# Optimization experiments

Measured on AMD Instinct MI355X. Metric: run time of the kernel, lower is better.

The kernel has to match this reference:

```python
import jax, jax.numpy as jnp
import numpy as np

N_MESH = 10242
N_GRID = 65160
N_EDGES = 195480
D = 512          # latent dim for mesh/grid nodes and edges
OUT = 471        # out_grid_node_dim
EDGE_IN = 4      # raw mesh2grid edge attribute dim


def _mlp(x, w0, b0, w1, b1):
    # MLP(in, hidden, out) with one hidden layer and SiLU (swish) activation, as in GraphCast
    return jax.nn.silu(x @ w0 + b0) @ w1 + b1


def setup_inputs() -> dict:
    key = jax.random.key(0)
    ks = jax.random.split(key, 24)
    s = 0.05  # weight scale to keep activations sane
    inp = {
        "mesh_node_features": jax.random.normal(ks[0], (1, N_MESH, D), jnp.float32),
        "grid_node_features": jax.random.normal(ks[1], (1, N_GRID, D), jnp.float32),
        "edge_attrs": jax.random.normal(ks[2], (N_EDGES, EDGE_IN), jnp.float32),
        "edge_src": jax.random.randint(ks[3], (N_EDGES,), 0, N_MESH),
        "edge_dst": jax.random.randint(ks[4], (N_EDGES,), 0, N_GRID),
        # edge embedder: 4 -> 512 -> 512
        "emb_w0": jax.random.normal(ks[5], (EDGE_IN, D)) * s,
        "emb_b0": jnp.zeros((D,)),
        "emb_w1": jax.random.normal(ks[6], (D, D)) * s,
        "emb_b1": jnp.zeros((D,)),
        # processor edge MLP: [src(512) + dst(512) + edge(512)] -> 512 -> 512
        "edge_w0": jax.random.normal(ks[7], (3 * D, D)) * s,
        "edge_b0": jnp.zeros((D,)),
        "edge_w1": jax.random.normal(ks[8], (D, D)) * s,
        "edge_b1": jnp.zeros((D,)),
        # processor node MLP: [grid(512) + agg(512)] -> 512 -> 512
        "node_w0": jax.random.normal(ks[9], (2 * D, D)) * s,
        "node_b0": jnp.zeros((D,)),
        "node_w1": jax.random.normal(ks[10], (D, D)) * s,
        "node_b1": jnp.zeros((D,)),
        # output MLP: 512 -> 512 -> 471
        "out_w0": jax.random.normal(ks[11], (D, D)) * s,
        "out_b0": jnp.zeros((D,)),
        "out_w1": jax.random.normal(ks[12], (D, OUT)) * s,
        "out_b1": jnp.zeros((OUT,)),
    }
    return inp


def reference(mesh_node_features, grid_node_features, edge_attrs, edge_src, edge_dst,
              emb_w0, emb_b0, emb_w1, emb_b1,
              edge_w0, edge_b0, edge_w1, edge_b1,
              node_w0, node_b0, node_w1, node_b1,
              out_w0, out_b0, out_w1, out_b1):
    B = grid_node_features.shape[0]
    # 1) embed raw edge attributes [E,4] -> [E,D]
    e = _mlp(edge_attrs, emb_w0, emb_b0, emb_w1, emb_b1)
    e = jnp.broadcast_to(e[None], (B, N_EDGES, D))  # [B,E,D]
    # 2) one message-passing step (InteractionNetwork style, residual)
    src = mesh_node_features[:, edge_src]  # gather: [B,E,D]
    dst = grid_node_features[:, edge_dst]  # gather: [B,E,D]
    e_in = jnp.concatenate([src, dst, e], axis=-1)  # [B,E,3D]
    e = e + _mlp(e_in, edge_w0, edge_b0, edge_w1, edge_b1)  # residual edge update
    # scatter-sum messages onto destination grid nodes
    agg = jax.vmap(lambda ef: jax.ops.segment_sum(ef, edge_dst, num_segments=N_GRID))(e)  # [B,N_GRID,D]
    n_in = jnp.concatenate([grid_node_features, agg], axis=-1)  # [B,N_GRID,2D]
    grid = grid_node_features + _mlp(n_in, node_w0, node_b0, node_w1, node_b1)  # residual node update
    # 3) output MLP (no layernorm)
    out = _mlp(grid, out_w0, out_b0, out_w1, out_b1)  # [B,N_GRID,OUT]
    return out.astype(jnp.float32)
```

## Files before the change

kernel.cpp:

```cpp
#include <hip/hip_runtime.h>
#include <stdint.h>

#define NE 195480
#define NM 10242
#define NG 65160
#define DD 512
#define NOUT 471

typedef __attribute__((ext_vector_type(8))) short bf16x8;
typedef __attribute__((ext_vector_type(4))) float f32x4;
typedef __attribute__((ext_vector_type(8))) unsigned short ushort8;

__device__ __forceinline__ float bf2f(unsigned short u) {
    union { unsigned int i; float f; } v; v.i = ((unsigned int)u) << 16; return v.f;
}
__device__ __forceinline__ unsigned short f2bf(float f) {
    union { float f; unsigned int u; } v; v.f = f;
    unsigned int x = v.u;
    return (unsigned short)((x + 0x7fffu + ((x >> 16) & 1u)) >> 16);
}
__device__ __forceinline__ float silu_f(float x) { return x / (1.f + __expf(-x)); }

__device__ __forceinline__ ushort8 cvt8(const float* __restrict__ p) {
    const f32x4 lo = *(const f32x4*)p;
    const f32x4 hi = *(const f32x4*)(p + 4);
    ushort8 r;
    #pragma unroll
    for (int j = 0; j < 4; ++j) { r[j] = f2bf(lo[j]); r[j + 4] = f2bf(hi[j]); }
    return r;
}

__device__ __forceinline__ void gl_lds16(const unsigned short* g, unsigned short* l) {
    __builtin_amdgcn_global_load_lds(
        (const __attribute__((address_space(1))) unsigned int*)g,
        (__attribute__((address_space(3))) unsigned int*)l, 16, 0, 0);
}

enum { A_PLAIN = 0, A_SEG = 1 };
enum { E_BIAS_BF16 = 0, E_SILU_BF16 = 1, E_AGGSILU = 2, E_OUT_F32 = 3 };

template<int AMODE, int EPI>
__global__ __launch_bounds__(256)
void gemm128(const unsigned short* __restrict__ Asrc,
             const unsigned short* __restrict__ Asrc2,
             const unsigned short* __restrict__ Asrc3,
             const unsigned short* __restrict__ Bw,
             const float* __restrict__ bias,
             const float* __restrict__ bias2,
             int M, int N, int K, int ldOut,
             const unsigned* __restrict__ degA,
             unsigned short* __restrict__ outB,
             float* __restrict__ outF)
{
    __shared__ unsigned short As[128 * 64];
    __shared__ unsigned short Bs[128 * 64];

    const int tid  = threadIdx.x;
    const int nwg  = gridDim.x;
    int orig = blockIdx.x;
    if ((nwg & 7) == 0) {
        const int q = nwg >> 3;
        orig = (blockIdx.x & 7) * q + (blockIdx.x >> 3);
    }
    const int bn = orig & 3;
    const int bm = orig >> 2;

    const int w    = tid >> 6;
    const int lane = tid & 63;
    const int quad = lane >> 4;
    const int ln   = lane & 15;
    const int wr   = w >> 1;
    const int wc   = w & 1;

    const int srow = tid >> 3;
    const int sc   = tid & 7;
    const int ck   = (sc ^ (srow & 7)) * 8;

    int arowc[4];
    #pragma unroll
    for (int i = 0; i < 4; ++i) {
        int r = bm * 128 + i * 32 + srow;
        arowc[i] = (r < M) ? r : (M - 1);
    }

    f32x4 acc[4][4] = {};

    for (int k0 = 0; k0 < K; k0 += 64) {
        __syncthreads();
        #pragma unroll
        for (int i = 0; i < 4; ++i) {
            const int row = i * 32 + srow;
            const unsigned short* ga;
            if (AMODE == A_PLAIN) {
                ga = Asrc + (size_t)arowc[i] * K + k0 + ck;
            } else {
                if (k0 < 512)       ga = Asrc  + (size_t)arowc[i] * 512 + k0 + ck;
                else if (k0 < 1024) ga = Asrc2 + (size_t)arowc[i] * 512 + (k0 - 512) + ck;
                else                ga = Asrc3 + (size_t)arowc[i] * 512 + (k0 - 1024) + ck;
            }
            gl_lds16(ga, As + i * 2048 + tid * 8);
            gl_lds16(Bw + (size_t)(bn * 128 + row) * K + k0 + ck, Bs + i * 2048 + tid * 8);
        }
        __syncthreads();

        #pragma unroll
        for (int kt = 0; kt < 2; ++kt) {
            bf16x8 af[4], bfv[4];
            #pragma unroll
            for (int m = 0; m < 4; ++m) {
                const int r = wr * 64 + m * 16 + ln;
                af[m] = *(const bf16x8*)(As + r * 64 + (((kt * 4 + quad) ^ (r & 7)) * 8));
            }
            #pragma unroll
            for (int n = 0; n < 4; ++n) {
                const int r = wc * 64 + n * 16 + ln;
                bfv[n] = *(const bf16x8*)(Bs + r * 64 + (((kt * 4 + quad) ^ (r & 7)) * 8));
            }
            #pragma unroll
            for (int m = 0; m < 4; ++m)
                #pragma unroll
                for (int n = 0; n < 4; ++n)
                    acc[m][n] = __builtin_amdgcn_mfma_f32_16x16x32_bf16(af[m], bfv[n], acc[m][n], 0, 0, 0);
        }
    }

    int colg[4]; float bcol[4], bcol2[4]; bool cok[4];
    #pragma unroll
    for (int n = 0; n < 4; ++n) {
        colg[n] = bn * 128 + wc * 64 + n * 16 + ln;
        cok[n]  = (colg[n] < N);
        bcol[n] = cok[n] ? bias[colg[n]] : 0.f;
        bcol2[n] = (EPI == E_AGGSILU && cok[n]) ? bias2[colg[n]] : 0.f;
    }
    #pragma unroll
    for (int m = 0; m < 4; ++m) {
        #pragma unroll
        for (int r = 0; r < 4; ++r) {
            const int row_g = bm * 128 + wr * 64 + m * 16 + quad * 4 + r;
            if (row_g >= M) continue;
            const float deg = (EPI == E_AGGSILU) ? (float)degA[row_g] : 0.f;
            #pragma unroll
            for (int n = 0; n < 4; ++n) {
                if (!cok[n]) continue;
                float v = acc[m][n][r] + bcol[n];
                if (EPI == E_BIAS_BF16) {
                    outB[(size_t)row_g * ldOut + colg[n]] = f2bf(v);
                } else if (EPI == E_SILU_BF16) {
                    outB[(size_t)row_g * ldOut + colg[n]] = f2bf(silu_f(v));
                } else if (EPI == E_AGGSILU) {
                    outB[(size_t)row_g * ldOut + colg[n]] = f2bf(silu_f(v + deg * bcol2[n]));
                } else {
                    outF[(size_t)row_g * N + colg[n]] = v;
                }
            }
        }
    }
}

__global__ __launch_bounds__(256)
void wconv(const float* __restrict__ w, unsigned short* __restrict__ wT,
           int K, int N, int Npad, int ldT)
{
    __shared__ float t[64][65];
    const int tid = threadIdx.x;
    const int bk = blockIdx.x * 64, bn = blockIdx.y * 64;
    const int cc = tid & 63, rr = tid >> 6;
    #pragma unroll
    for (int i = 0; i < 16; ++i) {
        const int k = rr + i * 4;
        float v = 0.f;
        if (bk + k < K && bn + cc < N) v = w[(size_t)(bk + k) * N + bn + cc];
        t[k][cc] = v;
    }
    __syncthreads();
    #pragma unroll
    for (int i = 0; i < 16; ++i) {
        const int n = rr + i * 4;
        if (bn + n < Npad && bk + cc < K)
            wT[(size_t)(bn + n) * ldT + bk + cc] = f2bf(t[cc][n]);
    }
}

__global__ __launch_bounds__(256)
void cvtb(const float* __restrict__ in, unsigned short* __restrict__ out, long long n8)
{
    const long long i = (long long)blockIdx.x * 256 + threadIdx.x;
    if (i >= n8) return;
    *(ushort8*)(out + i * 8) = cvt8(in + i * 8);
}

__global__ __launch_bounds__(256)
void embed_l1(const float* __restrict__ attrs,
              const float* __restrict__ w0,
              const float* __restrict__ b0,
              unsigned short* __restrict__ h)
{
    const long long idx = (long long)blockIdx.x * 256 + threadIdx.x;
    if (idx >= (long long)NE * 512) return;
    const int row = (int)(idx >> 9);
    const int c = (int)(idx & 511);
    float acc = b0[c];
    #pragma unroll
    for (int k = 0; k < 4; ++k)
        acc += attrs[row * 4 + k] * w0[k * 512 + c];
    h[idx] = f2bf(silu_f(acc));
}

__global__ __launch_bounds__(256)
void esilu(unsigned short* __restrict__ z,
           const unsigned short* __restrict__ mP,
           const unsigned short* __restrict__ gP,
           const int* __restrict__ esrc,
           const int* __restrict__ edst)
{
    const int row = blockIdx.x * 4 + (threadIdx.x >> 6);
    if (row >= NE) return;
    const int l8 = (threadIdx.x & 63) * 8;
    const int se = esrc[row], de = edst[row];
    ushort8 a = *(const ushort8*)(z  + (size_t)row * 512 + l8);
    ushort8 b = *(const ushort8*)(mP + (size_t)se  * 512 + l8);
    ushort8 c = *(const ushort8*)(gP + (size_t)de  * 512 + l8);
    ushort8 o;
    #pragma unroll
    for (int j = 0; j < 8; ++j)
        o[j] = f2bf(silu_f(bf2f(a[j]) + bf2f(b[j]) + bf2f(c[j])));
    *(ushort8*)(z + (size_t)row * 512 + l8) = o;
}

__global__ __launch_bounds__(256)
void fillslots(const int* __restrict__ edst, unsigned* __restrict__ fill,
               unsigned* __restrict__ slots)
{
    const int i = blockIdx.x * 256 + threadIdx.x;
    if (i >= NE) return;
    const int d = edst[i];
    const unsigned p = atomicAdd(&fill[d], 1u);
    if (p < 64u) slots[(size_t)d * 64 + p] = (unsigned)i;
}

__global__ __launch_bounds__(256)
void segsum2(const unsigned short* __restrict__ h1,
             const unsigned short* __restrict__ h3,
             const unsigned* __restrict__ fill,
             const unsigned* __restrict__ slots,
             unsigned short* __restrict__ s1,
             unsigned short* __restrict__ s3)
{
    const int g = blockIdx.x;
    const int c = threadIdx.x;
    unsigned deg = fill[g]; if (deg > 64u) deg = 64u;
    float a0 = 0.f, a1 = 0.f, b0 = 0.f, b1 = 0.f;
    for (unsigned j = 0; j < deg; ++j) {
        const size_t row = (size_t)slots[(size_t)g * 64 + j] * 512;
        a0 += bf2f(h1[row + c]);
        a1 += bf2f(h1[row + c + 256]);
        b0 += bf2f(h3[row + c]);
        b1 += bf2f(h3[row + c + 256]);
    }
    s1[(size_t)g * 512 + c]       = f2bf(a0);
    s1[(size_t)g * 512 + c + 256] = f2bf(a1);
    s3[(size_t)g * 512 + c]       = f2bf(b0);
    s3[(size_t)g * 512 + c + 256] = f2bf(b1);
}

__global__ __launch_bounds__(256)
void vmb(const float* __restrict__ base, const float* __restrict__ v1,
         const float* __restrict__ v2, const float* __restrict__ W,
         float* __restrict__ out)
{
    const int j = blockIdx.x * 256 + threadIdx.x;
    if (j >= 512) return;
    float a = base[j];
    for (int k = 0; k < 512; ++k) {
        float vk = v1[k] + (v2 ? v2[k] : 0.f);
        a += vk * W[(size_t)k * 512 + j];
    }
    out[j] = a;
}

extern "C" void kernel_launch(void* const* d_in, const int* in_sizes, int n_in,
                              void* d_out, int out_size, void* d_ws, size_t ws_size,
                              hipStream_t stream)
{
    const float* mesh    = (const float*)d_in[0];
    const float* gridf   = (const float*)d_in[1];
    const float* attrs   = (const float*)d_in[2];
    const int*   esrc    = (const int*)d_in[3];
    const int*   edst    = (const int*)d_in[4];
    const float* emb_w0  = (const float*)d_in[5];
    const float* emb_b0  = (const float*)d_in[6];
    const float* emb_w1  = (const float*)d_in[7];
    const float* emb_b1  = (const float*)d_in[8];
    const float* edge_w0 = (const float*)d_in[9];
    const float* edge_b0 = (const float*)d_in[10];
    const float* edge_w1 = (const float*)d_in[11];
    const float* edge_b1 = (const float*)d_in[12];
    const float* node_w0 = (const float*)d_in[13];
    const float* node_b0 = (const float*)d_in[14];
    const float* node_w1 = (const float*)d_in[15];
    const float* node_b1 = (const float*)d_in[16];
    const float* out_w0  = (const float*)d_in[17];
    const float* out_b0  = (const float*)d_in[18];
    const float* out_w1  = (const float*)d_in[19];
    const float* out_b1  = (const float*)d_in[20];

    char* ws = (char*)d_ws;
    unsigned short* h1  = (unsigned short*)ws;
    unsigned short* hb  = (unsigned short*)(ws + (size_t)NE * 512 * 2);
    char*           r3  = ws + (size_t)2 * NE * 512 * 2;
    unsigned short* hb5 = h1;
    unsigned short* gridP = (unsigned short*)r3;
    unsigned short* meshP = (unsigned short*)(r3 + 66723840);
    unsigned short* s1    = (unsigned short*)r3;
    unsigned short* s3    = (unsigned short*)(r3 + 66723840);
    unsigned short* out_w1T = (unsigned short*)r3;

    char* sc = (char*)d_out;
    unsigned short* BwG5     = (unsigned short*)sc;
    unsigned short* BwG7     = (unsigned short*)(sc +  1572864);
    unsigned short* W1T      = (unsigned short*)(sc +  2621440);
    unsigned short* W2T      = (unsigned short*)(sc +  3145728);
    unsigned short* W3T      = (unsigned short*)(sc +  3670016);
    unsigned short* WpT      = (unsigned short*)(sc +  4194304);
    unsigned short* nw0bT    = (unsigned short*)(sc +  4718592);
    unsigned short* ow0T     = (unsigned short*)(sc +  5242880);
    unsigned short* emb_w1b  = (unsigned short*)(sc +  5767168);
    unsigned short* edge_w1b = (unsigned short*)(sc +  6291456);
    unsigned short* node_w1b = (unsigned short*)(sc +  6815744);
    unsigned short* meshB    = (unsigned short*)(sc +  7340032);
    unsigned short* gridB    = (unsigned short*)(sc + 17827840);
    unsigned*       fillA    = (unsigned*)      (sc + 84551680);
    float*          zbias    = (float*)         (sc + 84812320);
    float*          bpp      = (float*)         (sc + 84814368);
    float*          c5       = (float*)         (sc + 84816416);
    float*          b7       = (float*)         (sc + 84818464);
    unsigned*       slots    = (unsigned*)      (sc + 84820512);

    hipMemsetAsync(fillA, 0, 260640 + 2048, stream);

    dim3 blk(256);
    { dim3 g(8, 8); wconv<<<g, blk, 0, stream>>>(edge_w0,                      W1T, 512, 512, 512,  512); }
    { dim3 g(8, 8); wconv<<<g, blk, 0, stream>>>(edge_w0 + (size_t) 512 * 512, W2T, 512, 512, 512,  512); }
    { dim3 g(8, 8); wconv<<<g, blk, 0, stream>>>(edge_w0 + (size_t)1024 * 512, W3T, 512, 512, 512,  512); }
    { dim3 g(8, 8); wconv<<<g, blk, 0, stream>>>(node_w0,                      BwG5, 512, 512, 512, 1536); }
    { dim3 g(8, 8); wconv<<<g, blk, 0, stream>>>(node_w0 + (size_t)512 * 512,  nw0bT, 512, 512, 512, 512); }
    { dim3 g(8, 8); wconv<<<g, blk, 0, stream>>>(out_w0,  ow0T, 512, 512, 512,  512); }
    { dim3 g(8, 8); wconv<<<g, blk, 0, stream>>>(out_w0,  BwG7, 512, 512, 512, 1024); }
    cvtb<<<128, blk, 0, stream>>>(emb_w1,  emb_w1b,  512 * 512 / 8);
    cvtb<<<128, blk, 0, stream>>>(edge_w1, edge_w1b, 512 * 512 / 8);
    cvtb<<<128, blk, 0, stream>>>(node_w1, node_w1b, 512 * 512 / 8);
    cvtb<<<(int)(((long long)NM * 512 / 8 + 255) / 256), blk, 0, stream>>>(mesh,  meshB, (long long)NM * 512 / 8);
    cvtb<<<(int)(((long long)NG * 512 / 8 + 255) / 256), blk, 0, stream>>>(gridf, gridB, (long long)NG * 512 / 8);
    fillslots<<<(NE + 255) / 256, blk, 0, stream>>>(edst, fillA, slots);
    vmb<<<2, blk, 0, stream>>>(edge_b0, emb_b1, nullptr, edge_w0 + (size_t)1024 * 512, bpp);
    vmb<<<2, blk, 0, stream>>>(zbias, emb_b1, edge_b1, node_w0 + (size_t)512 * 512, c5);
    vmb<<<2, blk, 0, stream>>>(out_b0, node_b1, nullptr, out_w0, b7);

    gemm128<A_PLAIN, E_BIAS_BF16><<<16, blk, 0, stream>>>(W3T, nullptr, nullptr, emb_w1b, zbias, nullptr,
        512, 512, 512, 512, nullptr, WpT, nullptr);
    gemm128<A_PLAIN, E_BIAS_BF16><<<16, blk, 0, stream>>>(nw0bT, nullptr, nullptr, emb_w1b, zbias, nullptr,
        512, 512, 512, 1536, nullptr, BwG5 + 512, nullptr);
    gemm128<A_PLAIN, E_BIAS_BF16><<<16, blk, 0, stream>>>(nw0bT, nullptr, nullptr, edge_w1b, zbias, nullptr,
        512, 512, 512, 1536, nullptr, BwG5 + 1024, nullptr);
    gemm128<A_PLAIN, E_BIAS_BF16><<<16, blk, 0, stream>>>(ow0T, nullptr, nullptr, node_w1b, zbias, nullptr,
        512, 512, 512, 1024, nullptr, BwG7 + 512, nullptr);

    embed_l1<<<(int)(((long long)NE * 512 + 255) / 256), blk, 0, stream>>>(attrs, emb_w0, emb_b0, h1);

    const int nwgE = 4 * ((NE + 127) / 128);
    const int nwgG = 4 * ((NG + 127) / 128);
    const int nwgM = 4 * ((NM + 127) / 128);

    gemm128<A_PLAIN, E_BIAS_BF16><<<nwgM, blk, 0, stream>>>(meshB, nullptr, nullptr, W1T, zbias, nullptr,
        NM, 512, 512, 512, nullptr, meshP, nullptr);
    gemm128<A_PLAIN, E_BIAS_BF16><<<nwgG, blk, 0, stream>>>(gridB, nullptr, nullptr, W2T, bpp, nullptr,
        NG, 512, 512, 512, nullptr, gridP, nullptr);

    gemm128<A_PLAIN, E_BIAS_BF16><<<nwgE, blk, 0, stream>>>(h1, nullptr, nullptr, WpT, zbias, nullptr,
        NE, 512, 512, 512, nullptr, hb, nullptr);
    esilu<<<(NE + 3) / 4, blk, 0, stream>>>(hb, meshP, gridP, esrc, edst);
    segsum2<<<NG, blk, 0, stream>>>(h1, hb, fillA, slots, s1, s3);
    gemm128<A_SEG, E_AGGSILU><<<nwgG, blk, 0, stream>>>(gridB, s1, s3, BwG5, node_b0, c5,
        NG, 512, 1536, 512, fillA, hb5, nullptr);
    { dim3 g(8, 8); wconv<<<g, blk, 0, stream>>>(out_w1, out_w1T, 512, 471, 512, 512); }
    gemm128<A_SEG, E_SILU_BF16><<<nwgG, blk, 0, stream>>>(gridB, hb5, nullptr, BwG7, b7, nullptr,
        NG, 512, 1024, 512, nullptr, hb, nullptr);
    gemm128<A_PLAIN, E_OUT_F32><<<nwgG, blk, 0, stream>>>(hb, nullptr, nullptr, out_w1T, out_b1, nullptr,
        NG, NOUT, 512, NOUT, nullptr, nullptr, (float*)d_out);
}
```

Measured before the change: 1.681 ms.

## Fuse edge silu and embedding recompute into segment-sum, vectorize embed layer

Removes the separate esilu pass by computing silu(z + meshP[src] + gridP[dst]) inside the per-node segment-sum. The first embedding layer is also recomputed there from the 4 raw attributes instead of re-reading the E×512 h1 buffer. The embed_l1 kernel now writes 8 bf16 values per thread. Buffers are reassigned so gridP and meshP reuse the h1 region after the edge GEMM has consumed it. This cuts several full passes over E×512 bf16 data, in exchange for more ALU work and scattered meshP gathers inside segsum.

```diff
diff --git a/kernel.cpp b/kernel.cpp
--- a/kernel.cpp
+++ b/kernel.cpp
@@ -195,36 +195,21 @@
               const float* __restrict__ b0,
               unsigned short* __restrict__ h)
 {
-    const long long idx = (long long)blockIdx.x * 256 + threadIdx.x;
-    if (idx >= (long long)NE * 512) return;
-    const int row = (int)(idx >> 9);
-    const int c = (int)(idx & 511);
-    float acc = b0[c];
-    #pragma unroll
-    for (int k = 0; k < 4; ++k)
-        acc += attrs[row * 4 + k] * w0[k * 512 + c];
-    h[idx] = f2bf(silu_f(acc));
-}
-
-__global__ __launch_bounds__(256)
-void esilu(unsigned short* __restrict__ z,
-           const unsigned short* __restrict__ mP,
-           const unsigned short* __restrict__ gP,
-           const int* __restrict__ esrc,
-           const int* __restrict__ edst)
-{
-    const int row = blockIdx.x * 4 + (threadIdx.x >> 6);
-    if (row >= NE) return;
-    const int l8 = (threadIdx.x & 63) * 8;
-    const int se = esrc[row], de = edst[row];
-    ushort8 a = *(const ushort8*)(z  + (size_t)row * 512 + l8);
-    ushort8 b = *(const ushort8*)(mP + (size_t)se  * 512 + l8);
-    ushort8 c = *(const ushort8*)(gP + (size_t)de  * 512 + l8);
+    const long long i = (long long)blockIdx.x * 256 + threadIdx.x;
+    if (i >= (long long)NE * 64) return;
+    const int row = (int)(i >> 6);
+    const int c8  = (int)(i & 63) * 8;
+    const float t0 = attrs[row * 4], t1 = attrs[row * 4 + 1];
+    const float t2 = attrs[row * 4 + 2], t3 = attrs[row * 4 + 3];
     ushort8 o;
     #pragma unroll
-    for (int j = 0; j < 8; ++j)
-        o[j] = f2bf(silu_f(bf2f(a[j]) + bf2f(b[j]) + bf2f(c[j])));
-    *(ushort8*)(z + (size_t)row * 512 + l8) = o;
+    for (int j = 0; j < 8; ++j) {
+        const int c = c8 + j;
+        float a = b0[c] + t0 * w0[c] + t1 * w0[512 + c]
+                + t2 * w0[1024 + c] + t3 * w0[1536 + c];
+        o[j] = f2bf(silu_f(a));
+    }
+    *(ushort8*)(h + (size_t)row * 512 + c8) = o;
 }
 
 __global__ __launch_bounds__(256)
@@ -239,8 +224,13 @@
 }
 
 __global__ __launch_bounds__(256)
-void segsum2(const unsigned short* __restrict__ h1,
-             const unsigned short* __restrict__ h3,
+void segsum3(const unsigned short* __restrict__ z3,
+             const unsigned short* __restrict__ mP,
+             const unsigned short* __restrict__ gP,
+             const float* __restrict__ attrs,
+             const float* __restrict__ w0,
+             const float* __restrict__ b0,
+             const int* __restrict__ esrc,
              const unsigned* __restrict__ fill,
              const unsigned* __restrict__ slots,
              unsigned short* __restrict__ s1,
@@ -249,18 +239,31 @@
     const int g = blockIdx.x;
     const int c = threadIdx.x;
     unsigned deg = fill[g]; if (deg > 64u) deg = 64u;
-    float a0 = 0.f, a1 = 0.f, b0 = 0.f, b1 = 0.f;
+    float w0a[4], w0b[4];
+    #pragma unroll
+    for (int k = 0; k < 4; ++k) { w0a[k] = w0[k * 512 + c]; w0b[k] = w0[k * 512 + c + 256]; }
+    const float b0a = b0[c], b0b = b0[c + 256];
+    const float gpa = bf2f(gP[(size_t)g * 512 + c]);
+    const float gpb = bf2f(gP[(size_t)g * 512 + c + 256]);
+    float a0 = 0.f, a1 = 0.f, q0 = 0.f, q1 = 0.f;
     for (unsigned j = 0; j < deg; ++j) {
-        const size_t row = (size_t)slots[(size_t)g * 64 + j] * 512;
-        a0 += bf2f(h1[row + c]);
-        a1 += bf2f(h1[row + c + 256]);
-        b0 += bf2f(h3[row + c]);
-        b1 += bf2f(h3[row + c + 256]);
+        const unsigned eid = slots[(size_t)g * 64 + j];
+        const int se = esrc[eid];
+        const float t0 = attrs[(size_t)eid * 4],     t1 = attrs[(size_t)eid * 4 + 1];
+        const float t2 = attrs[(size_t)eid * 4 + 2], t3 = attrs[(size_t)eid * 4 + 3];
+        a0 += silu_f(t0 * w0a[0] + t1 * w0a[1] + t2 * w0a[2] + t3 * w0a[3] + b0a);
+        a1 += silu_f(t0 * w0b[0] + t1 * w0b[1] + t2 * w0b[2] + t3 * w0b[3] + b0b);
+        const float za = bf2f(z3[(size_t)eid * 512 + c])
+                       + bf2f(mP[(size_t)se * 512 + c]) + gpa;
+        const float zb = bf2f(z3[(size_t)eid * 512 + c + 256])
+                       + bf2f(mP[(size_t)se * 512 + c + 256]) + gpb;
+        q0 += silu_f(za);
+        q1 += silu_f(zb);
     }
     s1[(size_t)g * 512 + c]       = f2bf(a0);
     s1[(size_t)g * 512 + c + 256] = f2bf(a1);
-    s3[(size_t)g * 512 + c]       = f2bf(b0);
-    s3[(size_t)g * 512 + c + 256] = f2bf(b1);
+    s3[(size_t)g * 512 + c]       = f2bf(q0);
+    s3[(size_t)g * 512 + c + 256] = f2bf(q1);
 }
 
 __global__ __launch_bounds__(256)
@@ -308,9 +311,9 @@
     unsigned short* h1  = (unsigned short*)ws;
     unsigned short* hb  = (unsigned short*)(ws + (size_t)NE * 512 * 2);
     char*           r3  = ws + (size_t)2 * NE * 512 * 2;
-    unsigned short* hb5 = h1;
-    unsigned short* gridP = (unsigned short*)r3;
-    unsigned short* meshP = (unsigned short*)(r3 + 66723840);
+    unsigned short* gridP = h1;
+    unsigned short* meshP = (unsigned short*)(ws + 66723840);
+    unsigned short* hb5   = h1;
     unsigned short* s1    = (unsigned short*)r3;
     unsigned short* s3    = (unsigned short*)(r3 + 66723840);
     unsigned short* out_w1T = (unsigned short*)r3;
@@ -365,21 +368,20 @@
     gemm128<A_PLAIN, E_BIAS_BF16><<<16, blk, 0, stream>>>(ow0T, nullptr, nullptr, node_w1b, zbias, nullptr,
         512, 512, 512, 1024, nullptr, BwG7 + 512, nullptr);
 
-    embed_l1<<<(int)(((long long)NE * 512 + 255) / 256), blk, 0, stream>>>(attrs, emb_w0, emb_b0, h1);
+    embed_l1<<<(int)(((long long)NE * 64 + 255) / 256), blk, 0, stream>>>(attrs, emb_w0, emb_b0, h1);
 
     const int nwgE = 4 * ((NE + 127) / 128);
     const int nwgG = 4 * ((NG + 127) / 128);
     const int nwgM = 4 * ((NM + 127) / 128);
 
+    gemm128<A_PLAIN, E_BIAS_BF16><<<nwgE, blk, 0, stream>>>(h1, nullptr, nullptr, WpT, zbias, nullptr,
+        NE, 512, 512, 512, nullptr, hb, nullptr);
+    gemm128<A_PLAIN, E_BIAS_BF16><<<nwgG, blk, 0, stream>>>(gridB, nullptr, nullptr, W2T, bpp, nullptr,
+        NG, 512, 512, 512, nullptr, gridP, nullptr);
     gemm128<A_PLAIN, E_BIAS_BF16><<<nwgM, blk, 0, stream>>>(meshB, nullptr, nullptr, W1T, zbias, nullptr,
         NM, 512, 512, 512, nullptr, meshP, nullptr);
-    gemm128<A_PLAIN, E_BIAS_BF16><<<nwgG, blk, 0, stream>>>(gridB, nullptr, nullptr, W2T, bpp, nullptr,
-        NG, 512, 512, 512, nullptr, gridP, nullptr);
-
-    gemm128<A_PLAIN, E_BIAS_BF16><<<nwgE, blk, 0, stream>>>(h1, nullptr, nullptr, WpT, zbias, nullptr,
-        NE, 512, 512, 512, nullptr, hb, nullptr);
-    esilu<<<(NE + 3) / 4, blk, 0, stream>>>(hb, meshP, gridP, esrc, edst);
-    segsum2<<<NG, blk, 0, stream>>>(h1, hb, fillA, slots, s1, s3);
+    segsum3<<<NG, blk, 0, stream>>>(hb, meshP, gridP, attrs, emb_w0, emb_b0,
+        esrc, fillA, slots, s1, s3);
     gemm128<A_SEG, E_AGGSILU><<<nwgG, blk, 0, stream>>>(gridB, s1, s3, BwG5, node_b0, c5,
         NG, 512, 1536, 512, fillA, hb5, nullptr);
     { dim3 g(8, 8); wconv<<<g, blk, 0, stream>>>(out_w1, out_w1T, 512, 471, 512, 512); }
```

Result: faster. 1.482 ms (-11.8%).
